# Kernel optimization log

Measured on AMD Instinct MI355X. Metric: run time of the kernel, lower is better.

The kernel has to match this reference:

```python
import jax, jax.numpy as jnp
import numpy as np

B, C, HH, WW = 256, 1024, 7, 7
S = HH * WW            # 49 tokens
D = 1024               # hidden_size
L = 2                  # encoder_layers (nhead arg, swapped in source)
H = 2                  # attention heads (num_layers arg, swapped in source)
HD = D // H            # 512 head dim
FF = 1024              # encoder_ffn_dim
OUT = 1024             # head output
EPS = 1e-5


def setup_inputs() -> dict:
    key = jax.random.key(0)
    ks = jax.random.split(key, 10)
    n = lambda k, shape: jax.random.normal(k, shape, jnp.float32) * 0.02
    return dict(
        x=jax.random.normal(ks[0], (B, C, HH, WW), jnp.float32),
        pos_emb=n(ks[1], (S, D)),
        ln1_s=jnp.ones((L, D), jnp.float32), ln1_b=jnp.zeros((L, D), jnp.float32),
        wq=n(ks[2], (L, D, D)), wk=n(ks[3], (L, D, D)),
        wv=n(ks[4], (L, D, D)), wo=n(ks[5], (L, D, D)),
        ln2_s=jnp.ones((L, D), jnp.float32), ln2_b=jnp.zeros((L, D), jnp.float32),
        w1=n(ks[6], (L, D, FF)), b1=jnp.zeros((L, FF), jnp.float32),
        w2=n(ks[7], (L, FF, D)), b2=jnp.zeros((L, D), jnp.float32),
        lnf_s=jnp.ones((D,), jnp.float32), lnf_b=jnp.zeros((D,), jnp.float32),
        head_w=n(ks[8], (S * D, OUT)), head_b=jnp.zeros((OUT,), jnp.float32),
    )


def _ln(x, s, b):
    m = jnp.mean(x, axis=-1, keepdims=True)
    v = jnp.var(x, axis=-1, keepdims=True)
    return (x - m) * jax.lax.rsqrt(v + EPS) * s + b


def reference(x, pos_emb, ln1_s, ln1_b, wq, wk, wv, wo, ln2_s, ln2_b,
              w1, b1, w2, b2, lnf_s, lnf_b, head_w, head_b):
    b = x.shape[0]
    # flatten HxW then permute -> [B, S, D] token sequence
    h = x.reshape(b, C, S).transpose(0, 2, 1)
    # BigBirdPegasus encoder: learned pos emb added to inputs_embeds (no scaling path)
    h = h + pos_emb[None, :, :]
    scale = 1.0 / jnp.sqrt(jnp.float32(HD))
    for i in range(L):
        # --- self-attention block (pre-LN); seq_len=49 triggers original_full attention ---
        r = h
        hn = _ln(h, ln1_s[i], ln1_b[i])
        q = (hn @ wq[i]).reshape(b, S, H, HD)
        k = (hn @ wk[i]).reshape(b, S, H, HD)
        v = (hn @ wv[i]).reshape(b, S, H, HD)
        scores = jnp.einsum('bqhd,bkhd->bhqk', q, k) * scale
        attn = jax.nn.softmax(scores, axis=-1)
        ctx = jnp.einsum('bhqk,bkhd->bqhd', attn, v).reshape(b, S, D)
        h = r + ctx @ wo[i]
        # --- feed-forward block (pre-LN, gelu_new) ---
        r = h
        hn = _ln(h, ln2_s[i], ln2_b[i])
        hn = jax.nn.gelu(hn @ w1[i] + b1[i], approximate=True)
        h = r + hn @ w2[i] + b2[i]
    # BigBirdPegasus applies layernorm_embedding AFTER the layer stack
    h = _ln(h, lnf_s, lnf_b)
    # flatten + linear + relu head
    out = jax.nn.relu(h.reshape(b, S * D) @ head_w + head_b)
    return out
```

## Files before the change

kernel.cpp:

```cpp
#include <hip/hip_runtime.h>
#include <hip/hip_bf16.h>
#include <stdint.h>

#define Bq 256
#define Sq 49
#define Dq 1024
#define Hq 2
#define HDq 512
#define Mq (Bq*Sq)
#define KHEADq (Sq*Dq)
#define STq 3072

typedef unsigned short u16;
typedef short bf16x8 __attribute__((ext_vector_type(8)));
typedef float f32x4 __attribute__((ext_vector_type(4)));

__device__ inline u16 f2bf(float f){
  union { float f; uint32_t u; } c; c.f = f;
  uint32_t r = c.u + 0x7FFFu + ((c.u >> 16) & 1u);
  return (u16)(r >> 16);
}
__device__ inline float bf2f(u16 h){
  union { uint32_t u; float f; } c; c.u = ((uint32_t)h) << 16;
  return c.f;
}

#define GLOAD_LDS16(gp, lp) \
  __builtin_amdgcn_global_load_lds((__attribute__((address_space(1))) void*)(gp), \
                                   (__attribute__((address_space(3))) void*)(lp), 16, 0, 0)
#define MFMA16(a,b,c) __builtin_amdgcn_mfma_f32_16x16x32_bf16(a,b,c,0,0,0)

__global__ __launch_bounds__(256) void setup_kernel(
    const float* __restrict__ x, const float* __restrict__ pos,
    u16* __restrict__ h, float2* __restrict__ pstat, u16* __restrict__ qkv,
    const float* __restrict__ wq, const float* __restrict__ wk,
    const float* __restrict__ wv, const float* __restrict__ wo,
    const float* __restrict__ w1, const float* __restrict__ w2,
    const float* __restrict__ ln1s, const float* __restrict__ ln1b,
    const float* __restrict__ ln2s, const float* __restrict__ ln2b,
    u16* __restrict__ wT, float* __restrict__ uvbuf)
{
  __shared__ __align__(16) float smem[6336];
  int bid = blockIdx.x;
  int tid = threadIdx.x;
  if(bid < 2048){
    float* t = smem;
    int b = bid >> 3, yy = bid & 7, c0 = yy*128;
    int lane = tid & 63, wave = tid >> 6;
    if(b == 0){
      uint4* pz = (uint4*)(qkv + (size_t)Mq*STq + (size_t)yy*6144);
      pz[tid] = make_uint4(0,0,0,0);
      pz[256+tid] = make_uint4(0,0,0,0);
      pz[512+tid] = make_uint4(0,0,0,0);
    }
    const float* xb = x + (size_t)b*(Dq*Sq) + (size_t)c0*Sq;
    #pragma unroll
    for(int i=0;i<32;i++){
      int cc = wave + i*4;
      if(lane < Sq) t[lane*129 + cc] = xb[(size_t)cc*Sq + lane];
    }
    __syncthreads();
    #pragma unroll
    for(int p=0;p<25;p++){
      int idx = p*256 + tid;
      int s = idx >> 7, cc = idx & 127;
      if(s < Sq){
        float hv = t[s*129 + cc] + pos[s*Dq + c0 + cc];
        h[((size_t)b*Sq + s)*Dq + c0 + cc] = f2bf(hv);
        t[s*129 + cc] = hv;
      }
    }
    __syncthreads();
    int r = tid >> 2, qd = tid & 3;
    if(r < Sq){
      float S=0.f, Q=0.f;
      for(int cc=qd; cc<128; cc+=4){ float vv = t[r*129+cc]; S+=vv; Q+=vv*vv; }
      S += __shfl_xor(S,1); Q += __shfl_xor(Q,1);
      S += __shfl_xor(S,2); Q += __shfl_xor(Q,2);
      if(qd==0){ float2 pp; pp.x=S; pp.y=Q; pstat[(size_t)yy*Mq + b*Sq + r] = pp; }
    }
  } else if(bid < 14336){
    int j = bid - 2048;
    int slot = j >> 10, jb = j & 1023;
    int k0 = (jb & 31)*32, n0 = (jb >> 5)*32;
    int l = slot / 6, jj = slot - l*6;
    const float* srcs[6] = {wq,wk,wv,wo,w1,w2};
    const float* in = srcs[jj] + (size_t)l*Dq*Dq;
    const float* sc = (jj<3) ? (ln1s + l*Dq) : (jj==4 ? (ln2s + l*Dq) : nullptr);
    u16* o = wT + (size_t)slot*Dq*Dq;
    float (*t)[33] = (float(*)[33])smem;
    int tx = tid & 31, ty = tid >> 5;
    #pragma unroll
    for(int i=0;i<4;i++) t[ty+8*i][tx] = in[(size_t)(k0+ty+8*i)*Dq + n0+tx];
    __syncthreads();
    float sck = sc ? sc[k0+tx] : 1.f;
    #pragma unroll
    for(int i=0;i<4;i++) o[(size_t)(n0+ty+8*i)*Dq + k0+tx] = f2bf(t[tx][ty+8*i] * sck);
  } else {
    int j = bid - 14336;
    float2 (*red)[32] = (float2(*)[32])smem;
    int t = tid;
    int colg = j*32 + (t & 31);
    int ks = t >> 5;
    int l = colg >> 12, col = colg & 4095;
    int jj = col >> 10, n = col & 1023;
    const float* srcs[4] = {wq, wk, wv, w1};
    const float* src = srcs[jj] + (size_t)l*Dq*Dq;
    const float* sc = (jj<3 ? ln1s : ln2s) + l*Dq;
    const float* bi = (jj<3 ? ln1b : ln2b) + l*Dq;
    float u=0.f, v=0.f;
    for(int k=ks*128;k<ks*128+128;k++){
      float val = src[(size_t)k*Dq + n];
      u += sc[k]*val; v += bi[k]*val;
    }
    float2 pp; pp.x=u; pp.y=v;
    red[ks][t&31] = pp;
    __syncthreads();
    if(t < 32){
      float U=0.f, V=0.f;
      #pragma unroll
      for(int s2=0;s2<8;s2++){ float2 q2 = red[s2][t]; U+=q2.x; V+=q2.y; }
      uvbuf[(size_t)(j*32 + t)*2]   = U;
      uvbuf[(size_t)(j*32 + t)*2+1] = V;
    }
  }
}

__global__ __launch_bounds__(256) void ln_kernel(const u16* __restrict__ hin,
    const float* __restrict__ sc, const float* __restrict__ bi, u16* __restrict__ outp){
  int wave = threadIdx.x >> 6, lane = threadIdx.x & 63;
  int row = blockIdx.x*4 + wave;
  const u16* p = hin + (size_t)row*Dq + lane*16;
  uint4 t0 = *(const uint4*)p;
  uint4 t1 = *(const uint4*)(p + 8);
  float v[16];
  {
    uint32_t wds[8] = {t0.x,t0.y,t0.z,t0.w,t1.x,t1.y,t1.z,t1.w};
    #pragma unroll
    for(int i=0;i<8;i++){
      v[2*i]   = bf2f((u16)(wds[i] & 0xffff));
      v[2*i+1] = bf2f((u16)(wds[i] >> 16));
    }
  }
  float s=0.f, sq=0.f;
  #pragma unroll
  for(int i=0;i<16;i++){ s += v[i]; sq += v[i]*v[i]; }
  #pragma unroll
  for(int o=32;o>=1;o>>=1){ s += __shfl_xor(s,o); sq += __shfl_xor(sq,o); }
  float mean = s * (1.f/Dq);
  float var  = sq * (1.f/Dq) - mean*mean;
  float rs = rsqrtf(var + 1e-5f);
  int c0 = lane*16;
  uint32_t w[8];
  #pragma unroll
  for(int i=0;i<8;i++){
    u16 lo = f2bf((v[2*i]   - mean)*rs*sc[c0+2*i]   + bi[c0+2*i]);
    u16 hi = f2bf((v[2*i+1] - mean)*rs*sc[c0+2*i+1] + bi[c0+2*i+1]);
    w[i] = (uint32_t)lo | ((uint32_t)hi << 16);
  }
  uint4* ob = (uint4*)(outp + (size_t)row*Dq + c0);
  ob[0] = make_uint4(w[0],w[1],w[2],w[3]);
  ob[1] = make_uint4(w[4],w[5],w[6],w[7]);
}

template<int EPI>
__global__ __launch_bounds__(512, 2) void gemm_nt2(
    const u16* __restrict__ A, int lda,
    const u16* __restrict__ Bt, int ldb,
    void* __restrict__ Cout, const u16* __restrict__ resid,
    const float* __restrict__ bias, int ldc,
    const float2* __restrict__ pstat_in, int nchunk,
    const float* __restrict__ uvp, float2* __restrict__ pstat_out,
    int total, int gxT)
{
  __shared__ u16 lds[65536];
  int tid = threadIdx.x, lane = tid & 63;
  int wave = tid >> 6;
  int wm = wave >> 2, wn = wave & 3;
  int l15 = lane & 15, l4 = lane >> 4;
  int swz = (l15 & 7) << 4;

  int srow = tid >> 3, scolb = (tid & 7) * 16;
  int scolx = scolb ^ ((srow & 7) << 4);

  for(int w = blockIdx.x; w < total; w += gridDim.x){
    int qq = total >> 3, rr = total & 7;
    int xcd = w & 7, idx = w >> 3;
    int wgid = (xcd < rr ? xcd*(qq+1) : rr*(qq+1) + (xcd-rr)*qq) + idx;
    int bx = wgid % gxT, by = wgid / gxT;
    int m0 = by*256, n0 = bx*256;

    auto stage2 = [&](int d, int kt, int h){
      #pragma unroll
      for(int cc=0; cc<2; cc++){
        int c = 2*h + cc;
        if(c < 4){
          int row = c*64 + srow;
          const u16* src = A + (size_t)(m0+row)*lda + kt*64 + (scolx>>1);
          GLOAD_LDS16(src, &lds[d*16384 + c*4096 + tid*8]);
        } else {
          int c4 = c - 4;
          int row = c4*64 + srow;
          const u16* src = Bt + (size_t)(n0+row)*ldb + kt*64 + (scolx>>1);
          GLOAD_LDS16(src, &lds[32768 + d*16384 + c4*4096 + tid*8]);
        }
      }
    };
    auto rdA = [&](int d, int i, int s)->bf16x8{
      int row = wm*128 + i*16 + l15;
      int byt = row*128 + ((s*64 + l4*16) ^ swz);
      return *(const bf16x8*)((const char*)lds + d*32768 + byt);
    };
    auto rdB = [&](int d, int n, int s)->bf16x8{
      int row = wn*64 + n*16 + l15;
      int byt = row*128 + ((s*64 + l4*16) ^ swz);
      return *(const bf16x8*)((const char*)lds + 65536 + d*32768 + byt);
    };

    f32x4 acc[8][4] = {};

    __syncthreads();
    #pragma unroll
    for(int h=0;h<4;h++) stage2(0, 0, h);

    for(int t=0; t<16; ++t){
      int d = t & 1;
      bf16x8 bfr[4][2];
      if(t < 15){
        stage2(d^1, t+1, 0);
        asm volatile("s_waitcnt vmcnt(2)" ::: "memory");
      } else {
        asm volatile("s_waitcnt vmcnt(0)" ::: "memory");
      }
      __builtin_amdgcn_sched_barrier(0);
      __builtin_amdgcn_s_barrier();
      bfr[0][0]=rdB(d,0,0); bfr[0][1]=rdB(d,0,1);
      bfr[1][0]=rdB(d,1,0); bfr[1][1]=rdB(d,1,1);
      bf16x8 a0s0=rdA(d,0,0), a0s1=rdA(d,0,1), a1s0=rdA(d,1,0), a1s1=rdA(d,1,1);
      __builtin_amdgcn_s_setprio(1);
      acc[0][0]=MFMA16(a0s0,bfr[0][0],acc[0][0]); acc[0][0]=MFMA16(a0s1,bfr[0][1],acc[0][0]);
      acc[0][1]=MFMA16(a0s0,bfr[1][0],acc[0][1]); acc[0][1]=MFMA16(a0s1,bfr[1][1],acc[0][1]);
      acc[1][0]=MFMA16(a1s0,bfr[0][0],acc[1][0]); acc[1][0]=MFMA16(a1s1,bfr[0][1],acc[1][0]);
      acc[1][1]=MFMA16(a1s0,bfr[1][0],acc[1][1]); acc[1][1]=MFMA16(a1s1,bfr[1][1],acc[1][1]);
      __builtin_amdgcn_s_setprio(0);
      __builtin_amdgcn_s_barrier();
      bfr[2][0]=rdB(d,2,0); bfr[2][1]=rdB(d,2,1);
      bfr[3][0]=rdB(d,3,0); bfr[3][1]=rdB(d,3,1);
      if(t < 15) stage2(d^1, t+1, 1);
      __builtin_amdgcn_s_barrier();
      __builtin_amdgcn_s_setprio(1);
      acc[0][2]=MFMA16(a0s0,bfr[2][0],acc[0][2]); acc[0][2]=MFMA16(a0s1,bfr[2][1],acc[0][2]);
      acc[0][3]=MFMA16(a0s0,bfr[3][0],acc[0][3]); acc[0][3]=MFMA16(a0s1,bfr[3][1],acc[0][3]);
      acc[1][2]=MFMA16(a1s0,bfr[2][0],acc[1][2]); acc[1][2]=MFMA16(a1s1,bfr[2][1],acc[1][2]);
      acc[1][3]=MFMA16(a1s0,bfr[3][0],acc[1][3]); acc[1][3]=MFMA16(a1s1,bfr[3][1],acc[1][3]);
      __builtin_amdgcn_s_setprio(0);
      __builtin_amdgcn_s_barrier();
      #pragma unroll
      for(int q=1;q<4;q++){
        bf16x8 c0s0=rdA(d,2*q,0), c0s1=rdA(d,2*q,1), c1s0=rdA(d,2*q+1,0), c1s1=rdA(d,2*q+1,1);
        if(t < 15 && q < 3) stage2(d^1, t+1, q+1);
        __builtin_amdgcn_s_barrier();
        __builtin_amdgcn_s_setprio(1);
        #pragma unroll
        for(int n=0;n<4;n++){
          acc[2*q][n]   = MFMA16(c0s0, bfr[n][0], acc[2*q][n]);
          acc[2*q][n]   = MFMA16(c0s1, bfr[n][1], acc[2*q][n]);
          acc[2*q+1][n] = MFMA16(c1s0, bfr[n][0], acc[2*q+1][n]);
          acc[2*q+1][n] = MFMA16(c1s1, bfr[n][1], acc[2*q+1][n]);
        }
        __builtin_amdgcn_s_setprio(0);
        __builtin_amdgcn_s_barrier();
      }
    }

    if constexpr (EPI == 1){
      float2* statsS = (float2*)((char*)lds + 49152);
      float* slotf = (float*)((char*)lds + wave*4096);
      float bv[4];
      #pragma unroll
      for(int n=0;n<4;n++) bv[n] = bias ? bias[n0 + wn*64 + n*16 + l15] : 0.f;
      #pragma unroll
      for(int i=0;i<8;i++){
        #pragma unroll
        for(int n=0;n<4;n++)
          #pragma unroll
          for(int r=0;r<4;r++)
            slotf[(l4*4+r)*64 + n*16 + l15] = acc[i][n][r] + bv[n];
        #pragma unroll
        for(int st=0;st<2;st++){
          int u = st*64 + lane;
          int row = u >> 3, c8 = (u & 7)*8;
          f32x4 lo = *(const f32x4*)&slotf[row*64 + c8];
          f32x4 hi = *(const f32x4*)&slotf[row*64 + c8 + 4];
          size_t o = (size_t)(m0 + wm*128 + i*16 + row)*ldc + n0 + wn*64 + c8;
          bf16x8 rb = *(const bf16x8*)(resid + o);
          bf16x8 ov; float fs=0.f, fq=0.f;
          #pragma unroll
          for(int j=0;j<4;j++){
            float a_ = lo[j] + bf2f((u16)rb[j]);
            float b_ = hi[j] + bf2f((u16)rb[4+j]);
            ov[j]   = (short)f2bf(a_);
            ov[4+j] = (short)f2bf(b_);
            fs += a_ + b_; fq += a_*a_ + b_*b_;
          }
          *(bf16x8*)((u16*)Cout + o) = ov;
          fs += __shfl_xor(fs,1); fq += __shfl_xor(fq,1);
          fs += __shfl_xor(fs,2); fq += __shfl_xor(fq,2);
          fs += __shfl_xor(fs,4); fq += __shfl_xor(fq,4);
          if((lane&7)==0){
            float2 pp; pp.x=fs; pp.y=fq;
            statsS[(wm*128 + i*16 + st*8 + (lane>>3))*4 + wn] = pp;
          }
        }
      }
      __syncthreads();
      if(tid < 256){
        float S=0.f, Q=0.f;
        #pragma unroll
        for(int w2_=0;w2_<4;w2_++){ float2 pp = statsS[tid*4+w2_]; S+=pp.x; Q+=pp.y; }
        float2 pp; pp.x=S; pp.y=Q;
        pstat_out[(size_t)bx*Mq + m0 + tid] = pp;
      }
    } else {
      float2* lstat = (float2*)((char*)lds + 49152);
      if(tid < 256){
        float S=0.f, Q=0.f;
        for(int c=0;c<nchunk;c++){ float2 pp = pstat_in[(size_t)c*Mq + m0 + tid]; S+=pp.x; Q+=pp.y; }
        float mean = S*(1.f/1024.f);
        float var  = Q*(1.f/1024.f) - mean*mean;
        float2 sm; sm.x = rsqrtf(var + 1e-5f); sm.y = mean;
        lstat[tid] = sm;
      }
      __syncthreads();
      u16* slot = (u16*)((char*)lds + wave*2048);
      float uvv[4][2], bv[4];
      #pragma unroll
      for(int n=0;n<4;n++){
        int ncol = n0 + wn*64 + n*16 + l15;
        float2 uv2 = ((const float2*)uvp)[ncol];
        uvv[n][0] = uv2.x; uvv[n][1] = uv2.y;
        if constexpr (EPI == 2) bv[n] = bias[ncol];
      }
      #pragma unroll
      for(int i=0;i<8;i++){
        #pragma unroll
        for(int n=0;n<4;n++)
          #pragma unroll
          for(int r=0;r<4;r++){
            float2 sm = lstat[wm*128 + i*16 + l4*4 + r];
            float va = sm.x*acc[i][n][r] - sm.x*sm.y*uvv[n][0] + uvv[n][1];
            u16 ov;
            if constexpr (EPI == 0){
              ov = f2bf(va);
            } else {
              float xg = va + bv[n];
              float tg = tanhf(0.79788456080286536f*(xg + 0.044715f*xg*xg*xg));
              ov = f2bf(0.5f*xg*(1.f+tg));
            }
            slot[(l4*4+r)*64 + n*16 + l15] = ov;
          }
        #pragma unroll
        for(int st=0;st<2;st++){
          int u = st*64 + lane;
          int row = u >> 3, c8 = (u & 7)*8;
          bf16x8 v8 = *(const bf16x8*)&slot[row*64 + c8];
          *(bf16x8*)((u16*)Cout + (size_t)(m0 + wm*128 + i*16 + row)*ldc + n0 + wn*64 + c8) = v8;
        }
      }
    }
  }
}

__global__ __launch_bounds__(256, 3) void gemm_head(
    const u16* __restrict__ A, const float* __restrict__ W,
    u16* __restrict__ parts)
{
  __shared__ u16 sA[2][128*32];
  int tid = threadIdx.x, lane = tid & 63;
  int wave = tid >> 6;
  int wm = wave >> 1, wn = wave & 1;
  int l15 = lane & 15, l4 = lane >> 4;
  int bx = blockIdx.x, by = blockIdx.y, z = blockIdx.z;
  int n0 = bx*128, m0 = by*128;
  size_t abase = (size_t)m0*KHEADq + (size_t)z*1024;
  f32x4 acc[4][4] = {};
  const float* wp = W + ((size_t)z*1024 + (size_t)l4*8)*1024 + n0 + wn*64 + l15;

  auto stageA = [&](int d, int kt){
    #pragma unroll
    for(int c=0;c<2;c++){
      int s2 = c*256+tid;
      GLOAD_LDS16(A + abase + (size_t)(s2>>2)*KHEADq + kt*32 + (s2&3)*8, &sA[d][s2*8]);
    }
  };
  float wA[4][8], wB[4][8];
  auto loadW = [&](float (&dst)[4][8], int kt){
    #pragma unroll
    for(int f=0;f<4;f++)
      #pragma unroll
      for(int jj=0;jj<8;jj++)
        dst[f][jj] = wp[(size_t)(kt*32+jj)*1024 + f*16];
  };
  auto compute = [&](int d, float (&wreg)[4][8]){
    bf16x8 bfr[4];
    #pragma unroll
    for(int f=0;f<4;f++){
      bf16x8 bv;
      #pragma unroll
      for(int jj=0;jj<8;jj++)
        bv[jj] = __builtin_bit_cast(short, __float2bfloat16(wreg[f][jj]));
      bfr[f] = bv;
    }
    bf16x8 af[4];
    #pragma unroll
    for(int i=0;i<4;i++)
      af[i] = *(const bf16x8*)&sA[d][(wm*64 + i*16 + l15)*32 + l4*8];
    #pragma unroll
    for(int i=0;i<4;i++)
      #pragma unroll
      for(int j=0;j<4;j++)
        acc[i][j] = MFMA16(af[i], bfr[j], acc[i][j]);
  };

  stageA(0, 0);
  loadW(wA, 0);
  for(int k2=0; k2<16; ++k2){
    int kt = 2*k2;
    stageA(1, kt+1);
    loadW(wB, kt+1);
    asm volatile("s_waitcnt vmcnt(34)" ::: "memory");
    __builtin_amdgcn_s_barrier();
    compute(0, wA);
    __builtin_amdgcn_s_barrier();
    if(k2 < 15){
      stageA(0, kt+2);
      loadW(wA, kt+2);
      asm volatile("s_waitcnt vmcnt(34)" ::: "memory");
    } else {
      asm volatile("s_waitcnt vmcnt(0)" ::: "memory");
    }
    __builtin_amdgcn_s_barrier();
    compute(1, wB);
    __builtin_amdgcn_s_barrier();
  }

  u16* slot = &sA[0][wave*1024];
  u16* base = parts + (size_t)z*(Bq*1024);
  #pragma unroll
  for(int i=0;i<4;i++){
    #pragma unroll
    for(int j=0;j<4;j++)
      #pragma unroll
      for(int rr=0;rr<4;rr++)
        slot[(l4*4+rr)*64 + j*16 + l15] = f2bf(acc[i][j][rr]);
    #pragma unroll
    for(int st=0;st<2;st++){
      int u = st*64 + lane;
      int row = u >> 3, c8 = (u & 7)*8;
      bf16x8 v8 = *(const bf16x8*)&slot[row*64 + c8];
      *(bf16x8*)(base + (size_t)(m0 + wm*64 + i*16 + row)*1024 + n0 + wn*64 + c8) = v8;
    }
  }
}

__global__ __launch_bounds__(256) void attn_kernel(u16* __restrict__ qkv)
{
  __shared__ float sS[64][65];
  __shared__ u16 sP[64][64];
  __shared__ __align__(16) u16 sV[64*260 + 4];
  int bh = blockIdx.x;
  int b = bh >> 1, h = bh & 1;
  int tid = threadIdx.x, lane = tid & 63, wave = tid >> 6;
  int l15 = lane & 15, l4 = lane >> 4;
  f32x4 zero4 = {0.f,0.f,0.f,0.f};
  bf16x8 zb = {0,0,0,0,0,0,0,0};
  f32x4 acc[4];
  #pragma unroll
  for(int i=0;i<4;i++) acc[i] = zero4;
  int srow = wave*16 + l15;
  const u16* qp = qkv + (size_t)(b*Sq + srow)*STq + h*HDq + l4*8;
  const u16* kbase = qkv + (size_t)b*Sq*STq + Dq + h*HDq + l4*8;
  for(int kt=0;kt<16;kt++){
    bf16x8 aq = (srow < Sq) ? *(const bf16x8*)(qp + kt*32) : zb;
    #pragma unroll
    for(int fn=0;fn<4;fn++){
      int s2 = fn*16 + l15;
      bf16x8 bk = (s2 < Sq) ? *(const bf16x8*)(kbase + (size_t)s2*STq + kt*32) : zb;
      acc[fn] = MFMA16(aq, bk, acc[fn]);
    }
  }
  const float scale = 0.04419417382415922f;
  #pragma unroll
  for(int fn=0;fn<4;fn++)
    #pragma unroll
    for(int r=0;r<4;r++)
      sS[wave*16 + l4*4 + r][fn*16 + l15] = acc[fn][r]*scale;
  const u16* vsrc = qkv + (size_t)b*Sq*STq + 2*Dq + h*HDq;
  #pragma unroll
  for(int p=0;p<16;p++){
    int i = p*256 + tid;
    int row = i >> 6, ch = i & 63;
    uint2 v2 = (row < Sq) ? *(const uint2*)(vsrc + (size_t)row*STq + ch*4) : make_uint2(0u,0u);
    *(uint2*)&sV[row*260 + ch*4] = v2;
  }
  __syncthreads();
  {
    int r = tid >> 2, qd = tid & 3;
    float mx = -1e30f;
    for(int j=qd;j<Sq;j+=4) mx = fmaxf(mx, sS[r][j]);
    mx = fmaxf(mx, __shfl_xor(mx,1));
    mx = fmaxf(mx, __shfl_xor(mx,2));
    float sum = 0.f;
    for(int j=qd;j<Sq;j+=4){ float e = __expf(sS[r][j]-mx); sS[r][j]=e; sum+=e; }
    sum += __shfl_xor(sum,1);
    sum += __shfl_xor(sum,2);
    float inv = 1.f/sum;
    for(int j=qd;j<64;j+=4) sP[r][j] = (j<Sq)? f2bf(sS[r][j]*inv) : (u16)0;
  }
  uint2 vreg[16];
  #pragma unroll
  for(int p=0;p<16;p++){
    int i = p*256 + tid;
    int row = i >> 6, ch = i & 63;
    vreg[p] = (row < Sq) ? *(const uint2*)(vsrc + 256 + (size_t)row*STq + ch*4) : make_uint2(0u,0u);
  }
  __syncthreads();
  bf16x8 ap[2];
  #pragma unroll
  for(int kt2=0;kt2<2;kt2++)
    ap[kt2] = *(const bf16x8*)&sP[wave*16 + l15][kt2*32 + l4*8];
  u16* cb = qkv + (size_t)b*Sq*STq + h*HDq;
  for(int fn=0;fn<16;fn++){
    f32x4 c4 = zero4;
    #pragma unroll
    for(int kt2=0;kt2<2;kt2++){
      int rbase = kt2*32 + l4*8;
      bf16x8 bv;
      #pragma unroll
      for(int jj=0;jj<8;jj++) bv[jj] = (short)sV[(rbase+jj)*260 + fn*16 + l15];
      c4 = MFMA16(ap[kt2], bv, c4);
    }
    #pragma unroll
    for(int r=0;r<4;r++){
      int s = wave*16 + l4*4 + r;
      if(s < Sq) cb[(size_t)s*STq + fn*16 + l15] = f2bf(c4[r]);
    }
  }
  __syncthreads();
  #pragma unroll
  for(int p=0;p<16;p++){
    int i = p*256 + tid;
    int row = i >> 6, ch = i & 63;
    *(uint2*)&sV[row*260 + ch*4] = vreg[p];
  }
  __syncthreads();
  for(int fn=16;fn<32;fn++){
    f32x4 c4 = zero4;
    #pragma unroll
    for(int kt2=0;kt2<2;kt2++){
      int rbase = kt2*32 + l4*8;
      bf16x8 bv;
      #pragma unroll
      for(int jj=0;jj<8;jj++) bv[jj] = (short)sV[(rbase+jj)*260 + (fn-16)*16 + l15];
      c4 = MFMA16(ap[kt2], bv, c4);
    }
    #pragma unroll
    for(int r=0;r<4;r++){
      int s = wave*16 + l4*4 + r;
      if(s < Sq) cb[(size_t)s*STq + fn*16 + l15] = f2bf(c4[r]);
    }
  }
}

__global__ __launch_bounds__(256) void head_finalize(const u16* __restrict__ parts,
    const float* __restrict__ hb, float* __restrict__ outp){
  int idx = blockIdx.x*256 + threadIdx.x;
  float s = hb[idx & 1023];
  #pragma unroll
  for(int z=0;z<49;z++) s += bf2f(parts[(size_t)z*(Bq*1024) + idx]);
  outp[idx] = fmaxf(s, 0.f);
}

extern "C" void kernel_launch(void* const* d_in, const int* in_sizes, int n_in,
                              void* d_out, int out_size, void* d_ws, size_t ws_size,
                              hipStream_t stream) {
  (void)in_sizes; (void)n_in; (void)out_size;
  const float* x    = (const float*)d_in[0];
  const float* pos  = (const float*)d_in[1];
  const float* ln1s = (const float*)d_in[2];
  const float* ln1b = (const float*)d_in[3];
  const float* wq   = (const float*)d_in[4];
  const float* wk   = (const float*)d_in[5];
  const float* wv   = (const float*)d_in[6];
  const float* wo   = (const float*)d_in[7];
  const float* ln2s = (const float*)d_in[8];
  const float* ln2b = (const float*)d_in[9];
  const float* w1   = (const float*)d_in[10];
  const float* b1   = (const float*)d_in[11];
  const float* w2   = (const float*)d_in[12];
  const float* b2   = (const float*)d_in[13];
  const float* lnfs = (const float*)d_in[14];
  const float* lnfb = (const float*)d_in[15];
  const float* hw   = (const float*)d_in[16];
  const float* hb   = (const float*)d_in[17];
  float* out = (float*)d_out;

  char* ws = (char*)d_ws;
  size_t off = 0;
  auto carve = [&](size_t n) -> char* { char* p = ws + off; off += (n + 255) & ~(size_t)255; return p; };
  u16*   h     = (u16*)  carve((size_t)Mq*Dq*2);
  u16*   act0  = (u16*)  carve((size_t)Mq*Dq*2);
  u16*   act1  = (u16*)  carve((size_t)Mq*Dq*2);
  u16*   qkv   = (u16*)  carve((size_t)(Mq+16)*STq*2);
  u16*   wT    = (u16*)  carve((size_t)12*Dq*Dq*2);
  float2* pstat= (float2*)carve((size_t)8*Mq*sizeof(float2));
  float* uvbuf = (float*)carve((size_t)2*4096*2*4);
  u16*   parts = qkv;
  if (off > ws_size) return;

  setup_kernel<<<14592, 256, 0, stream>>>(x, pos, h, pstat, qkv,
      wq, wk, wv, wo, w1, w2, ln1s, ln1b, ln2s, ln2b, wT, uvbuf);

  for(int l=0;l<2;l++){
    u16* qkvT = wT + (size_t)(l*6+0)*Dq*Dq;
    u16* woT  = wT + (size_t)(l*6+3)*Dq*Dq;
    u16* w1T  = wT + (size_t)(l*6+4)*Dq*Dq;
    u16* w2T  = wT + (size_t)(l*6+5)*Dq*Dq;
    const float* uvq = uvbuf + (size_t)l*8192;
    const float* uv1 = uvbuf + (size_t)l*8192 + 3072*2;

    gemm_nt2<0><<<512, 512, 0, stream>>>(h, Dq, qkvT, Dq, qkv, nullptr, nullptr, STq,
                                         pstat, (l==0)?8:4, uvq, nullptr, 588, 12);
    attn_kernel<<<Bq*Hq, 256, 0, stream>>>(qkv);
    gemm_nt2<1><<<196, 512, 0, stream>>>(qkv, STq, woT, Dq, h, h, nullptr, Dq,
                                         nullptr, 0, nullptr, pstat, 196, 4);
    gemm_nt2<2><<<196, 512, 0, stream>>>(h, Dq, w1T, Dq, act1, nullptr, b1 + l*Dq, Dq,
                                         pstat, 4, uv1, nullptr, 196, 4);
    gemm_nt2<1><<<196, 512, 0, stream>>>(act1, Dq, w2T, Dq, h, h, b2 + l*Dq, Dq,
                                         nullptr, 0, nullptr, pstat, 196, 4);
  }

  ln_kernel<<<Mq/4, 256, 0, stream>>>(h, lnfs, lnfb, act0);
  gemm_head<<<dim3(8,2,49), 256, 0, stream>>>(act0, hw, parts);
  head_finalize<<<1024, 256, 0, stream>>>(parts, hb, out);
}
```

Baseline: 670.7 us.

## Fuse final layernorm into head GEMM A-tile staging using precomputed row stats

Removes the standalone final layernorm kernel and its intermediate buffer. The head GEMM now reads the residual stream directly into registers, normalizes each element using per-row statistics reduced from partial sums written by the previous GEMM epilogue, and writes the result into LDS. This saves one full read and write pass over the activations and one kernel launch. In exchange, the A path moves from direct global-to-LDS loads to register staging, and the k-loop gains extra full barriers and ALU work.

```diff
diff --git a/kernel.cpp b/kernel.cpp
--- a/kernel.cpp
+++ b/kernel.cpp
@@ -124,43 +124,6 @@
       uvbuf[(size_t)(j*32 + t)*2+1] = V;
     }
   }
-}
-
-__global__ __launch_bounds__(256) void ln_kernel(const u16* __restrict__ hin,
-    const float* __restrict__ sc, const float* __restrict__ bi, u16* __restrict__ outp){
-  int wave = threadIdx.x >> 6, lane = threadIdx.x & 63;
-  int row = blockIdx.x*4 + wave;
-  const u16* p = hin + (size_t)row*Dq + lane*16;
-  uint4 t0 = *(const uint4*)p;
-  uint4 t1 = *(const uint4*)(p + 8);
-  float v[16];
-  {
-    uint32_t wds[8] = {t0.x,t0.y,t0.z,t0.w,t1.x,t1.y,t1.z,t1.w};
-    #pragma unroll
-    for(int i=0;i<8;i++){
-      v[2*i]   = bf2f((u16)(wds[i] & 0xffff));
-      v[2*i+1] = bf2f((u16)(wds[i] >> 16));
-    }
-  }
-  float s=0.f, sq=0.f;
-  #pragma unroll
-  for(int i=0;i<16;i++){ s += v[i]; sq += v[i]*v[i]; }
-  #pragma unroll
-  for(int o=32;o>=1;o>>=1){ s += __shfl_xor(s,o); sq += __shfl_xor(sq,o); }
-  float mean = s * (1.f/Dq);
-  float var  = sq * (1.f/Dq) - mean*mean;
-  float rs = rsqrtf(var + 1e-5f);
-  int c0 = lane*16;
-  uint32_t w[8];
-  #pragma unroll
-  for(int i=0;i<8;i++){
-    u16 lo = f2bf((v[2*i]   - mean)*rs*sc[c0+2*i]   + bi[c0+2*i]);
-    u16 hi = f2bf((v[2*i+1] - mean)*rs*sc[c0+2*i+1] + bi[c0+2*i+1]);
-    w[i] = (uint32_t)lo | ((uint32_t)hi << 16);
-  }
-  uint4* ob = (uint4*)(outp + (size_t)row*Dq + c0);
-  ob[0] = make_uint4(w[0],w[1],w[2],w[3]);
-  ob[1] = make_uint4(w[4],w[5],w[6],w[7]);
 }
 
 template<int EPI>
@@ -373,25 +336,48 @@
 
 __global__ __launch_bounds__(256, 3) void gemm_head(
     const u16* __restrict__ A, const float* __restrict__ W,
+    const float2* __restrict__ pstat,
+    const float* __restrict__ lnfs, const float* __restrict__ lnfb,
     u16* __restrict__ parts)
 {
   __shared__ u16 sA[2][128*32];
+  __shared__ float2 slf[1024];
+  __shared__ float2 sLN[128];
   int tid = threadIdx.x, lane = tid & 63;
   int wave = tid >> 6;
   int wm = wave >> 1, wn = wave & 1;
   int l15 = lane & 15, l4 = lane >> 4;
   int bx = blockIdx.x, by = blockIdx.y, z = blockIdx.z;
   int n0 = bx*128, m0 = by*128;
-  size_t abase = (size_t)m0*KHEADq + (size_t)z*1024;
   f32x4 acc[4][4] = {};
   const float* wp = W + ((size_t)z*1024 + (size_t)l4*8)*1024 + n0 + wn*64 + l15;
 
-  auto stageA = [&](int d, int kt){
-    #pragma unroll
-    for(int c=0;c<2;c++){
-      int s2 = c*256+tid;
-      GLOAD_LDS16(A + abase + (size_t)(s2>>2)*KHEADq + kt*32 + (s2&3)*8, &sA[d][s2*8]);
-    }
+  if(tid < 128){
+    float S=0.f, Q=0.f;
+    #pragma unroll
+    for(int c=0;c<4;c++){ float2 pp = pstat[(size_t)c*Mq + (size_t)(m0+tid)*Sq + z]; S+=pp.x; Q+=pp.y; }
+    float mean = S*(1.f/1024.f);
+    float var  = Q*(1.f/1024.f) - mean*mean;
+    float2 sm; sm.x = rsqrtf(var + 1e-5f); sm.y = mean;
+    sLN[tid] = sm;
+  }
+  #pragma unroll
+  for(int p=0;p<4;p++){
+    int i = p*256 + tid;
+    float2 lf; lf.x = lnfs[i]; lf.y = lnfb[i];
+    slf[i] = lf;
+  }
+  __syncthreads();
+  float2 st0 = sLN[tid>>2];
+  float2 st1 = sLN[64 + (tid>>2)];
+  int acol = (tid & 3)*8;
+  const u16* a0p = A + ((size_t)(m0 + (tid>>2))*Sq + z)*Dq + acol;
+  const u16* a1p = A + ((size_t)(m0 + 64 + (tid>>2))*Sq + z)*Dq + acol;
+
+  uint4 aA[2], aB[2];
+  auto loadA = [&](uint4 (&dst)[2], int kt){
+    dst[0] = *(const uint4*)(a0p + kt*32);
+    dst[1] = *(const uint4*)(a1p + kt*32);
   };
   float wA[4][8], wB[4][8];
   auto loadW = [&](float (&dst)[4][8], int kt){
@@ -401,6 +387,25 @@
       for(int jj=0;jj<8;jj++)
         dst[f][jj] = wp[(size_t)(kt*32+jj)*1024 + f*16];
   };
+  auto lnwrite = [&](int d, uint4 (&src)[2], int kt){
+    #pragma unroll
+    for(int c=0;c<2;c++){
+      float2 st = c ? st1 : st0;
+      int s2 = c*256 + tid;
+      uint32_t wds[4] = {src[c].x, src[c].y, src[c].z, src[c].w};
+      u16 outv[8];
+      #pragma unroll
+      for(int j=0;j<4;j++){
+        float2 lf0 = slf[kt*32 + acol + 2*j];
+        float2 lf1 = slf[kt*32 + acol + 2*j + 1];
+        float v0 = (bf2f((u16)(wds[j] & 0xffff)) - st.y)*st.x;
+        float v1 = (bf2f((u16)(wds[j] >> 16))    - st.y)*st.x;
+        outv[2*j]   = f2bf(v0*lf0.x + lf0.y);
+        outv[2*j+1] = f2bf(v1*lf1.x + lf1.y);
+      }
+      *(uint4*)&sA[d][s2*8] = *(uint4*)outv;
+    }
+  };
   auto compute = [&](int d, float (&wreg)[4][8]){
     bf16x8 bfr[4];
     #pragma unroll
@@ -422,28 +427,35 @@
         acc[i][j] = MFMA16(af[i], bfr[j], acc[i][j]);
   };
 
-  stageA(0, 0);
-  loadW(wA, 0);
+  loadA(aA, 0); loadW(wA, 0);
+  asm volatile("s_waitcnt vmcnt(32)" ::: "memory");
+  lnwrite(0, aA, 0);
+  __syncthreads();
   for(int k2=0; k2<16; ++k2){
     int kt = 2*k2;
-    stageA(1, kt+1);
-    loadW(wB, kt+1);
+    loadA(aB, kt+1); loadW(wB, kt+1);
     asm volatile("s_waitcnt vmcnt(34)" ::: "memory");
-    __builtin_amdgcn_s_barrier();
     compute(0, wA);
-    __builtin_amdgcn_s_barrier();
+    asm volatile("s_waitcnt vmcnt(32)" ::: "memory");
+    __syncthreads();
+    lnwrite(1, aB, kt+1);
+    __syncthreads();
     if(k2 < 15){
-      stageA(0, kt+2);
-      loadW(wA, kt+2);
+      loadA(aA, kt+2); loadW(wA, kt+2);
       asm volatile("s_waitcnt vmcnt(34)" ::: "memory");
     } else {
       asm volatile("s_waitcnt vmcnt(0)" ::: "memory");
     }
-    __builtin_amdgcn_s_barrier();
     compute(1, wB);
-    __builtin_amdgcn_s_barrier();
-  }
-
+    if(k2 < 15){
+      asm volatile("s_waitcnt vmcnt(32)" ::: "memory");
+      __syncthreads();
+      lnwrite(0, aA, kt+2);
+      __syncthreads();
+    }
+  }
+
+  __syncthreads();
   u16* slot = &sA[0][wave*1024];
   u16* base = parts + (size_t)z*(Bq*1024);
   #pragma unroll
@@ -609,7 +621,6 @@
   size_t off = 0;
   auto carve = [&](size_t n) -> char* { char* p = ws + off; off += (n + 255) & ~(size_t)255; return p; };
   u16*   h     = (u16*)  carve((size_t)Mq*Dq*2);
-  u16*   act0  = (u16*)  carve((size_t)Mq*Dq*2);
   u16*   act1  = (u16*)  carve((size_t)Mq*Dq*2);
   u16*   qkv   = (u16*)  carve((size_t)(Mq+16)*STq*2);
   u16*   wT    = (u16*)  carve((size_t)12*Dq*Dq*2);
@@ -640,7 +651,6 @@
                                          nullptr, 0, nullptr, pstat, 196, 4);
   }
 
-  ln_kernel<<<Mq/4, 256, 0, stream>>>(h, lnfs, lnfb, act0);
-  gemm_head<<<dim3(8,2,49), 256, 0, stream>>>(act0, hw, parts);
+  gemm_head<<<dim3(8,2,49), 256, 0, stream>>>(h, hw, pstat, lnfs, lnfb, parts);
   head_finalize<<<1024, 256, 0, stream>>>(parts, hb, out);
 }
```

Result: slower. 686.0 us (+2.3%).
